# Optimization experiments

Hardware: AMD Instinct MI355X
Metric: run time of the kernel (lower is better)

The kernel has to match this reference:

```python
import jax, jax.numpy as jnp
import numpy as np

N = 100000          # num nodes
E = 1600000         # num edges (before self loops)
IN_C = 128
OUT_C = 64
RATIO = 0.5
NEG_SLOPE = 0.2


def setup_inputs() -> dict:
    key = jax.random.key(0)
    k1, k2, k3, k4, k5 = jax.random.split(key, 5)
    x = jax.random.normal(k1, (N, IN_C), jnp.float32)
    # edges with no self loops (module removes then re-adds self loops)
    src = jax.random.randint(k2, (E,), 0, N, dtype=jnp.int32)
    off = jax.random.randint(k3, (E,), 1, N, dtype=jnp.int32)
    tgt = (src + off) % N
    edge_index = jnp.stack([src, tgt])  # [2, E], row0=source(j), row1=target(i)
    # glorot init
    s_w = float(np.sqrt(6.0 / (IN_C + OUT_C)))
    weight = jax.random.uniform(k4, (IN_C, OUT_C), jnp.float32, -s_w, s_w)
    s_a = float(np.sqrt(6.0 / (1 + 2 * OUT_C)))
    att = jax.random.uniform(k5, (1, 2 * OUT_C), jnp.float32, -s_a, s_a)
    batch = jnp.zeros((N,), jnp.int32)  # single graph
    return {"x": x, "weight": weight, "att": att,
            "edge_index": edge_index, "batch": batch, "bn": 0}


def reference(x, weight, att, edge_index, batch, bn):
    # add self loops (static shapes: E + N edges)
    loops = jnp.arange(N, dtype=edge_index.dtype)
    src = jnp.concatenate([edge_index[0], loops])  # edge_index_j (source)
    tgt = jnp.concatenate([edge_index[1], loops])  # edge_index_i (target)

    h = x @ weight                      # [N, OUT_C]
    x_j = h[src]                        # [E+N, OUT_C] gathered source feats
    x_i = h[tgt]

    # alpha = (cat([x_i, x_j]) * att).sum(-1)
    alpha = x_i @ att[0, :OUT_C] + x_j @ att[0, OUT_C:]   # [E+N]
    alpha = jnp.where(alpha > 0, alpha, NEG_SLOPE * alpha)  # leaky_relu

    # edge-softmax grouped by target node (every node has a self loop -> no empty segment)
    m = jax.ops.segment_max(alpha, tgt, num_segments=N)
    a = jnp.exp(alpha - m[tgt])
    denom = jax.ops.segment_sum(a, tgt, num_segments=N)
    alpha = a / (denom[tgt] + 1e-16)

    # node importance = sum of attention over outgoing edges (grouped by source)
    alpha_sum = jax.ops.segment_sum(alpha, src, num_segments=N)

    # topk node selection (ratio of all nodes; single graph)
    k = int(np.ceil(RATIO * N))
    _, topk_idx = jax.lax.top_k(alpha_sum, k)
    node_mask = jnp.zeros((N,), bool).at[topk_idx].set(True)

    # filter_dn: keep edges whose both endpoints survive; mask instead of compacting
    edge_mask = node_mask[src] & node_mask[tgt]
    alpha_m = jnp.where(edge_mask, alpha, 0.0)

    # weighted scatter-add aggregation to target nodes (aggr='add')
    out = jax.ops.segment_sum(alpha_m[:, None] * x_j, tgt, num_segments=N)  # [N, OUT_C]
    # bn flag is 0 -> BatchNorm skipped
    return out, edge_mask, node_mask
```

## Files before the change

kernel.cpp:

```cpp
#include <hip/hip_runtime.h>
#include <stdint.h>

#define IN_C 128
#define OUT_C 64
#define NEG_SLOPE 0.2f
#define RB 256
#define RBINS 512
#define STAGE 8192
#define NGH (RBINS * RB)
#define NGHS (RBINS * RBINS)
#define KC 8
#define SXW 192

typedef unsigned int u32;
typedef unsigned long long u64;

__device__ __forceinline__ u32 fenc(float f) {
  u32 u = __float_as_uint(f);
  return (u & 0x80000000u) ? ~u : (u | 0x80000000u);
}
__device__ __forceinline__ u64 key64(float v, int i) {
  return (((u64)fenc(v)) << 32) | (u64)(0xffffffffu - (u32)i);
}

__global__ __launch_bounds__(128) void k_gemm(const float* __restrict__ x,
                                              const float* __restrict__ w,
                                              const float* __restrict__ att,
                                              float* __restrict__ h,
                                              float* __restrict__ ai, float* __restrict__ aj,
                                              int N) {
  __shared__ float sw[IN_C * OUT_C];
  __shared__ float sx[KC * SXW];
  int tid = threadIdx.x;
  int rbase = blockIdx.x * 128;

  for (int i = tid; i < (IN_C * OUT_C) / 4; i += 128)
    ((float4*)sw)[i] = ((const float4*)w)[i];

  int c0 = (tid & 7) * 8;
  int rg = tid >> 3;
  int sxbase = rg * 12;
  float acc[8][8];
#pragma unroll
  for (int i = 0; i < 8; i++)
#pragma unroll
    for (int j = 0; j < 8; j++) acc[i][j] = 0.f;

  int grow = rbase + tid;
  int base = (tid >> 3) * 12 + (tid & 7);
  const float* xp = &x[(size_t)grow * IN_C];

  float4 pv0 = make_float4(0.f, 0.f, 0.f, 0.f);
  float4 pv1 = make_float4(0.f, 0.f, 0.f, 0.f);
  if (grow < N) {
    pv0 = *(const float4*)&xp[0];
    pv1 = *(const float4*)&xp[4];
  }

  for (int kb = 0; kb < IN_C; kb += KC) {
    __syncthreads();
    sx[0 * SXW + base] = pv0.x;
    sx[1 * SXW + base] = pv0.y;
    sx[2 * SXW + base] = pv0.z;
    sx[3 * SXW + base] = pv0.w;
    sx[4 * SXW + base] = pv1.x;
    sx[5 * SXW + base] = pv1.y;
    sx[6 * SXW + base] = pv1.z;
    sx[7 * SXW + base] = pv1.w;
    if (kb + KC < IN_C && grow < N) {
      pv0 = *(const float4*)&xp[kb + KC];
      pv1 = *(const float4*)&xp[kb + KC + 4];
    }
    __syncthreads();
#pragma unroll
    for (int kl = 0; kl < KC; ++kl) {
      int kg = kb + kl;
      float xr[8], wv[8];
      *(float4*)&xr[0] = *(const float4*)&sx[kl * SXW + sxbase];
      *(float4*)&xr[4] = *(const float4*)&sx[kl * SXW + sxbase + 4];
      *(float4*)&wv[0] = *(const float4*)&sw[kg * OUT_C + c0];
      *(float4*)&wv[4] = *(const float4*)&sw[kg * OUT_C + c0 + 4];
#pragma unroll
      for (int i = 0; i < 8; ++i)
#pragma unroll
        for (int j = 0; j < 8; ++j)
          acc[i][j] += xr[i] * wv[j];
    }
  }

  float pi[8], pj[8];
#pragma unroll
  for (int i = 0; i < 8; ++i) { pi[i] = 0.f; pj[i] = 0.f; }
#pragma unroll
  for (int j = 0; j < 8; ++j) {
    float a0 = att[c0 + j], a1 = att[OUT_C + c0 + j];
#pragma unroll
    for (int i = 0; i < 8; ++i) {
      pi[i] += acc[i][j] * a0;
      pj[i] += acc[i][j] * a1;
    }
  }
#pragma unroll
  for (int o = 1; o < 8; o <<= 1) {
#pragma unroll
    for (int i = 0; i < 8; ++i) {
      pi[i] += __shfl_xor(pi[i], o);
      pj[i] += __shfl_xor(pj[i], o);
    }
  }
#pragma unroll
  for (int i = 0; i < 8; ++i) {
    int row = rbase + rg * 8 + i;
    if (row < N) {
      *(float4*)&h[(size_t)row * OUT_C + c0]     = make_float4(acc[i][0], acc[i][1], acc[i][2], acc[i][3]);
      *(float4*)&h[(size_t)row * OUT_C + c0 + 4] = make_float4(acc[i][4], acc[i][5], acc[i][6], acc[i][7]);
      if ((tid & 7) == 0) { ai[row] = pi[i]; aj[row] = pj[i]; }
    }
  }
}

__global__ __launch_bounds__(256) void k_rhist_t(const int* __restrict__ tgt,
                                                 int E, int EN, int chunk, u32* __restrict__ gh,
                                                 u32* __restrict__ hist8, u32* __restrict__ done,
                                                 u32* __restrict__ sel, u32* __restrict__ cnt, u32 k) {
  __shared__ u32 lh[RBINS];
  int tid = threadIdx.x, b = blockIdx.x;
  if (b == 0) {
    for (int i = tid; i < 2048; i += 256) hist8[i] = 0u;
    if (tid < 8) { done[tid] = 0u; cnt[tid] = 0u; }
    if (tid == 0) { sel[0] = 0u; sel[1] = 0u; sel[2] = k; sel[3] = 0u; }
  }
  for (int d = tid; d < RBINS; d += 256) lh[d] = 0u;
  __syncthreads();
  int lo = b * chunk, hi = min(lo + chunk, EN);
  for (int e = lo + tid; e < hi; e += 256) {
    int t = (e < E) ? tgt[e] : e - E;
    atomicAdd(&lh[((u32)t) >> 8], 1u);
  }
  __syncthreads();
  for (int d = tid; d < RBINS; d += 256) gh[d * RB + b] = lh[d];
}

__global__ __launch_bounds__(256) void k_scanA(const u32* __restrict__ in, u32* __restrict__ out,
                                               u32* __restrict__ bsum, int n) {
  __shared__ u32 s[256];
  int i = blockIdx.x * 256 + threadIdx.x;
  u32 v = (i < n) ? in[i] : 0u;
  s[threadIdx.x] = v;
  __syncthreads();
  for (int o = 1; o < 256; o <<= 1) {
    u32 t = (threadIdx.x >= (unsigned)o) ? s[threadIdx.x - o] : 0u;
    __syncthreads();
    s[threadIdx.x] += t;
    __syncthreads();
  }
  if (i < n) out[i] = s[threadIdx.x] - v;
  if (threadIdx.x == 255) bsum[blockIdx.x] = s[255];
}

__global__ __launch_bounds__(1024) void k_scanB(u32* __restrict__ bsum, int nb) {
  __shared__ u32 s[1024];
  int tid = threadIdx.x;
  u32 v = (tid < nb) ? bsum[tid] : 0u;
  s[tid] = v;
  __syncthreads();
  for (int o = 1; o < 1024; o <<= 1) {
    u32 t = (tid >= o) ? s[tid - o] : 0u;
    __syncthreads();
    s[tid] += t;
    __syncthreads();
  }
  if (tid < nb) bsum[tid] = s[tid] - v;
}

__global__ __launch_bounds__(256) void k_scanC(u32* __restrict__ out, const u32* __restrict__ bsum, int n) {
  int i = blockIdx.x * 256 + threadIdx.x;
  if (i < n) out[i] += bsum[blockIdx.x];
}

__global__ __launch_bounds__(256) void k_rscatter_t(const int* __restrict__ src, const int* __restrict__ tgt,
                                                    int E, int EN, int chunk,
                                                    const u32* __restrict__ gh, u32* __restrict__ bufB) {
  __shared__ u32 cnt[RBINS];
  int tid = threadIdx.x, b = blockIdx.x;
  for (int d = tid; d < RBINS; d += 256) cnt[d] = gh[d * RB + b];
  __syncthreads();
  int lo = b * chunk, hi = min(lo + chunk, EN);
  for (int e = lo + tid; e < hi; e += 256) {
    int s, t;
    if (e < E) { s = src[e]; t = tgt[e]; } else { s = t = e - E; }
    u32 p = atomicAdd(&cnt[((u32)t) >> 8], 1u);
    bufB[p] = (((u32)t & 255u) << 24) | (u32)s;
  }
}

__global__ __launch_bounds__(256) void k_rpass2(const u32* __restrict__ in, u32* __restrict__ out,
                                                const u32* __restrict__ gh, u32* __restrict__ ghs,
                                                u32* __restrict__ offT,
                                                const float* __restrict__ ai, const float* __restrict__ aj,
                                                float* __restrict__ alpha,
                                                int N, int EN) {
  __shared__ u32 hist[256];
  __shared__ u32 sc[256];
  __shared__ u32 lhs[RBINS];
  __shared__ u32 stage[STAGE];
  int tid = threadIdx.x, d = blockIdx.x;
  u32 start = gh[d * RB];
  u32 end = (d < RBINS - 1) ? gh[(d + 1) * RB] : (u32)EN;
  int sz = (int)(end - start);
  hist[tid] = 0u;
  for (int dd = tid; dd < RBINS; dd += 256) lhs[dd] = 0u;
  __syncthreads();
  for (u32 p = start + tid; p < end; p += 256) {
    u32 it = in[p];
    atomicAdd(&hist[it >> 24], 1u);
    atomicAdd(&lhs[(it & 0xffffffu) >> 8], 1u);
  }
  __syncthreads();
  for (int dd = tid; dd < RBINS; dd += 256) ghs[dd * RBINS + d] = lhs[dd];
  u32 hv = hist[tid];
  sc[tid] = hv;
  __syncthreads();
  for (int o = 1; o < 256; o <<= 1) {
    u32 t = (tid >= o) ? sc[tid - o] : 0u;
    __syncthreads();
    sc[tid] += t;
    __syncthreads();
  }
  u32 excl = sc[tid] - hv;
  int node = (d << 8) + tid;
  if (node < N) offT[node] = start + excl;
  if (node == 0) offT[N] = (u32)EN;
  hist[tid] = excl;
  __syncthreads();
  bool staged = (sz <= STAGE);
  for (u32 p = start + tid; p < end; p += 256) {
    u32 it = in[p];
    u32 lp = atomicAdd(&hist[it >> 24], 1u);
    if (staged) stage[lp] = it;
    else out[start + lp] = it;
  }
  __syncthreads();
  if (staged)
    for (int i = tid; i < sz; i += 256) out[start + i] = stage[i];
  __syncthreads();
  if (node < N) {
    int lb = (tid > 0) ? (int)sc[tid - 1] : 0;
    int le = (int)sc[tid];
    float an = ai[node];
    float mx = -1e30f;
    for (int i = lb; i < le; ++i) {
      u32 it = staged ? stage[i] : out[start + i];
      float a = an + aj[it & 0xffffffu];
      a = a > 0.f ? a : NEG_SLOPE * a;
      mx = fmaxf(mx, a);
      if (staged) stage[i] = __float_as_uint(a);
    }
    float sm = 0.f;
    for (int i = lb; i < le; ++i) {
      float a;
      if (staged) a = __uint_as_float(stage[i]);
      else {
        u32 it = out[start + i];
        a = an + aj[it & 0xffffffu];
        a = a > 0.f ? a : NEG_SLOPE * a;
      }
      float v = expf(a - mx);
      sm += v;
      if (staged) stage[i] = __float_as_uint(v);
      else alpha[start + i] = v;
    }
    float inv = 1.f / (sm + 1e-16f);
    for (int i = lb; i < le; ++i) {
      float v = staged ? __uint_as_float(stage[i]) : alpha[start + i];
      alpha[start + i] = v * inv;
    }
  }
}

__global__ __launch_bounds__(256) void k_rscatter_s(const u32* __restrict__ csr,
                                                    const float* __restrict__ alpha,
                                                    const u32* __restrict__ gh, const u32* __restrict__ ghs,
                                                    u64* __restrict__ bufB, int EN) {
  __shared__ u32 cnt[RBINS];
  int tid = threadIdx.x, d = blockIdx.x;
  for (int dd = tid; dd < RBINS; dd += 256) cnt[dd] = ghs[dd * RBINS + d];
  __syncthreads();
  u32 start = gh[d * RB];
  u32 end = (d < RBINS - 1) ? gh[(d + 1) * RB] : (u32)EN;
  for (u32 e = start + tid; e < end; e += 256) {
    u32 s = csr[e] & 0xffffffu;
    u32 p = atomicAdd(&cnt[s >> 8], 1u);
    bufB[p] = (((u64)(s & 255u)) << 32) | __float_as_uint(alpha[e]);
  }
}

__global__ __launch_bounds__(256) void k_asum_acc(const u64* __restrict__ bufB,
                                                  const u32* __restrict__ ghs,
                                                  float* __restrict__ asum, int N, int EN) {
  __shared__ float sums[256];
  int tid = threadIdx.x, d = blockIdx.x;
  u32 start = ghs[d * RBINS];
  u32 end = (d < RBINS - 1) ? ghs[(d + 1) * RBINS] : (u32)EN;
  sums[tid] = 0.f;
  __syncthreads();
  for (u32 p = start + tid; p < end; p += 256) {
    u64 it = bufB[p];
    atomicAdd(&sums[(u32)(it >> 32)], __uint_as_float((u32)it));
  }
  __syncthreads();
  int node = d * 256 + tid;
  if (node < N) asum[node] = sums[tid];
}

__global__ __launch_bounds__(256) void k_histpick(const float* __restrict__ asum,
                                                  const u32* __restrict__ list_in, const u32* __restrict__ cnt_in,
                                                  u32* __restrict__ list_out, u32* __restrict__ cnt_out,
                                                  u32* __restrict__ hist8, u32* __restrict__ done,
                                                  u32* __restrict__ sel, int N, int pass, int nblk) {
  __shared__ u32 lh[256];
  __shared__ u32 sres;
  __shared__ u32 s[256];
  int tid = threadIdx.x;
  lh[tid] = 0u;
  __syncthreads();
  u64 prefix = ((const u64*)sel)[0];
  int shift = 56 - 8 * pass;
  int n = list_in ? (int)*cnt_in : N;
  int i = blockIdx.x * 256 + tid;
  if (i < n) {
    int idx = list_in ? (int)list_in[i] : i;
    u64 k = key64(asum[idx], idx);
    bool ok = (pass == 0) || ((k >> (shift + 8)) == prefix);
    if (ok) {
      atomicAdd(&lh[(u32)(k >> shift) & 255u], 1u);
      if (list_out) {
        u32 p = atomicAdd(cnt_out, 1u);
        list_out[p] = (u32)idx;
      }
    }
  }
  __syncthreads();
  if (lh[tid]) atomicAdd(&hist8[pass * 256 + tid], lh[tid]);
  __syncthreads();
  if (tid == 0)
    sres = __hip_atomic_fetch_add(&done[pass], 1u, __ATOMIC_ACQ_REL, __HIP_MEMORY_SCOPE_AGENT);
  __syncthreads();
  if (sres == (u32)(nblk - 1)) {
    u32 krem = sel[2];
    u32 hv = __hip_atomic_load(&hist8[pass * 256 + (255 - tid)], __ATOMIC_RELAXED,
                               __HIP_MEMORY_SCOPE_AGENT);
    s[tid] = hv;
    __syncthreads();
    for (int o = 1; o < 256; o <<= 1) {
      u32 t = (tid >= o) ? s[tid - o] : 0u;
      __syncthreads();
      s[tid] += t;
      __syncthreads();
    }
    u32 cum = s[tid], prev = (tid > 0) ? s[tid - 1] : 0u;
    if (cum >= krem && prev < krem) {
      int dsel = 255 - tid;
      ((u64*)sel)[0] = (prefix << 8) | (u64)(u32)dsel;
      sel[2] = krem - prev;
    }
  }
}

__global__ __launch_bounds__(256) void k_finish(const float* __restrict__ asum,
                                                const u32* __restrict__ list, const u32* __restrict__ cntp,
                                                u32* __restrict__ sel) {
  __shared__ u64 keys[2048];
  __shared__ u32 cc;
  int tid = threadIdx.x;
  if (tid == 0) cc = 0u;
  __syncthreads();
  int n = (int)*cntp;
  u32 fsel = (u32)((const u64*)sel)[0];
  u32 krem = sel[2];
  for (int i = tid; i < n; i += 256) {
    int idx = (int)list[i];
    u64 k = key64(asum[idx], idx);
    if ((u32)(k >> 32) == fsel) {
      u32 p = atomicAdd(&cc, 1u);
      if (p < 2048) keys[p] = k;
    }
  }
  __syncthreads();
  int C = (int)min(cc, 2048u);
  for (int i = tid; i < C; i += 256) {
    u64 k = keys[i];
    u32 rank = 0;
    for (int j = 0; j < C; ++j)
      if (keys[j] > k) rank++;
    if (rank == krem - 1) ((u64*)sel)[0] = k;
  }
}

__global__ __launch_bounds__(256) void k_node_mask(const float* __restrict__ asum,
                                                   const u32* __restrict__ sel,
                                                   u32* __restrict__ nm,
                                                   float* __restrict__ out_node, int N) {
  int i = blockIdx.x * 256 + threadIdx.x;
  if (i >= N) return;
  u64 T = ((const u64*)sel)[0];
  bool m = key64(asum[i], i) >= T;
  nm[i] = m ? 1u : 0u;
  out_node[i] = m ? 1.f : 0.f;
}

__global__ __launch_bounds__(256) void k_mask(const int* __restrict__ src, const int* __restrict__ tgt,
                                              const u32* __restrict__ nm,
                                              const u32* __restrict__ csr, const float* __restrict__ alpha,
                                              float* __restrict__ out_edge, u64* __restrict__ pair,
                                              int E, int EN) {
  int e = blockIdx.x * 256 + threadIdx.x;
  if (e >= EN) return;
  int s, t;
  if (e < E) { s = src[e]; t = tgt[e]; } else { s = t = e - E; }
  out_edge[e] = (nm[s] && nm[t]) ? 1.f : 0.f;
  u32 sp = csr[e] & 0xffffffu;
  u32 ab = nm[sp] ? __float_as_uint(alpha[e]) : 0u;
  pair[e] = (((u64)sp) << 32) | ab;
}

__global__ __launch_bounds__(256) void k_aggregate(const u32* __restrict__ off,
                                                   const u64* __restrict__ pair,
                                                   const float* __restrict__ h,
                                                   const u32* __restrict__ nm,
                                                   float* __restrict__ out, int N) {
  int node = blockIdx.x * 4 + (threadIdx.x >> 6);
  int lane = threadIdx.x & 63;
  int g = lane >> 4;
  int c = lane & 15;
  if (node >= N) return;
  float4 acc = make_float4(0.f, 0.f, 0.f, 0.f);
  if (nm[node]) {
    u32 b = off[node], e2 = off[node + 1];
    for (u32 p0 = b; p0 < e2; p0 += 16) {
      u64 pr[4];
      float av[4];
      u32 sv[4];
#pragma unroll
      for (int q = 0; q < 4; ++q) {
        u32 p = p0 + q * 4 + (u32)g;
        bool ok = p < e2;
        pr[q] = pair[ok ? p : b];
        av[q] = ok ? __uint_as_float((u32)pr[q]) : 0.f;
        sv[q] = (u32)(pr[q] >> 32);
      }
      float4 hv[4];
#pragma unroll
      for (int q = 0; q < 4; ++q)
        hv[q] = *(const float4*)&h[(size_t)sv[q] * OUT_C + c * 4];
#pragma unroll
      for (int q = 0; q < 4; ++q) {
        acc.x += av[q] * hv[q].x;
        acc.y += av[q] * hv[q].y;
        acc.z += av[q] * hv[q].z;
        acc.w += av[q] * hv[q].w;
      }
    }
#pragma unroll
    for (int o = 16; o < 64; o <<= 1) {
      acc.x += __shfl_xor(acc.x, o);
      acc.y += __shfl_xor(acc.y, o);
      acc.z += __shfl_xor(acc.z, o);
      acc.w += __shfl_xor(acc.w, o);
    }
  }
  if (g == 0)
    *(float4*)&out[(size_t)node * OUT_C + c * 4] = acc;
}

extern "C" void kernel_launch(void* const* d_in, const int* in_sizes, int n_in,
                              void* d_out, int out_size, void* d_ws, size_t ws_size,
                              hipStream_t stream) {
  const float* x   = (const float*)d_in[0];
  const float* w   = (const float*)d_in[1];
  const float* att = (const float*)d_in[2];
  const int*   ei  = (const int*)d_in[3];

  int N = in_sizes[0] / IN_C;
  int E = in_sizes[3] / 2;
  int EN = E + N;
  const int* src = ei;
  const int* tgt = ei + E;

  float* out      = (float*)d_out;
  float* out_edge = out + (size_t)N * OUT_C;
  float* out_node = out_edge + (size_t)EN;

  char* p = (char*)d_ws;
  auto alloc = [&](size_t bytes) -> char* {
    char* r = p;
    p += (bytes + 255) & ~(size_t)255;
    return r;
  };
  float* h     = (float*)alloc((size_t)N * OUT_C * 4);
  float* ai    = (float*)alloc((size_t)N * 4);
  float* aj    = (float*)alloc((size_t)N * 4);
  u32*   bufA  = (u32*)alloc((size_t)EN * 4);
  u64*   bufB  = (u64*)alloc((size_t)EN * 8);
  float* alpha = (float*)alloc((size_t)EN * 4);
  u32*   offT  = (u32*)alloc((size_t)(N + 1) * 4);
  u32*   gh    = (u32*)alloc((size_t)NGH * 4);
  u32*   ghs   = (u32*)alloc((size_t)NGHS * 4);
  u32*   bsum  = (u32*)alloc(2048 * 4);
  float* asum  = (float*)alloc((size_t)N * 4);
  u32*   nm    = (u32*)alloc((size_t)N * 4);
  u32*   hist8 = (u32*)alloc(2048 * 4);
  u32*   done  = (u32*)alloc(8 * 4);
  u32*   cnt   = (u32*)alloc(8 * 4);
  u32*   sel   = (u32*)alloc(256);
  u32*   listA = (u32*)alloc((size_t)N * 4);
  u32*   listB = (u32*)alloc((size_t)N * 4);

  u32 kSel = (u32)((N + 1) / 2);
  int chunk = (EN + RB - 1) / RB;
  int nScanT = (NGH + 255) / 256;
  int nScanS = (NGHS + 255) / 256;
  int gGemm = (N + 127) / 128;
  int gN = (N + 255) / 256;
  int gE = (EN + 255) / 256;
  int gNode4 = (N + 3) / 4;

  k_gemm<<<gGemm, 128, 0, stream>>>(x, w, att, h, ai, aj, N);

  k_rhist_t<<<RB, 256, 0, stream>>>(tgt, E, EN, chunk, gh, hist8, done, sel, cnt, kSel);
  k_scanA<<<nScanT, 256, 0, stream>>>(gh, gh, bsum, NGH);
  k_scanB<<<1, 1024, 0, stream>>>(bsum, nScanT);
  k_scanC<<<nScanT, 256, 0, stream>>>(gh, bsum, NGH);
  k_rscatter_t<<<RB, 256, 0, stream>>>(src, tgt, E, EN, chunk, gh, (u32*)bufB);
  k_rpass2<<<RBINS, 256, 0, stream>>>((u32*)bufB, bufA, gh, ghs, offT, ai, aj, alpha, N, EN);

  k_scanA<<<nScanS, 256, 0, stream>>>(ghs, ghs, bsum, NGHS);
  k_scanB<<<1, 1024, 0, stream>>>(bsum, nScanS);
  k_scanC<<<nScanS, 256, 0, stream>>>(ghs, bsum, NGHS);
  k_rscatter_s<<<RBINS, 256, 0, stream>>>(bufA, alpha, gh, ghs, bufB, EN);
  k_asum_acc<<<RBINS, 256, 0, stream>>>(bufB, ghs, asum, N, EN);

  k_histpick<<<gN, 256, 0, stream>>>(asum, nullptr, nullptr, nullptr, nullptr,
                                     hist8, done, sel, N, 0, gN);
  k_histpick<<<gN, 256, 0, stream>>>(asum, nullptr, nullptr, listA, &cnt[1],
                                     hist8, done, sel, N, 1, gN);
  k_histpick<<<gN, 256, 0, stream>>>(asum, listA, &cnt[1], listB, &cnt[2],
                                     hist8, done, sel, N, 2, gN);
  k_histpick<<<gN, 256, 0, stream>>>(asum, listB, &cnt[2], listA, &cnt[3],
                                     hist8, done, sel, N, 3, gN);
  k_finish<<<1, 256, 0, stream>>>(asum, listA, &cnt[3], sel);

  k_node_mask<<<gN, 256, 0, stream>>>(asum, sel, nm, out_node, N);
  k_mask<<<gE, 256, 0, stream>>>(src, tgt, nm, bufA, alpha, out_edge, bufB, E, EN);
  k_aggregate<<<gNode4, 256, 0, stream>>>(offT, bufB, h, nm, out, N);
}
```

Before: 365.6 us.

## Replace source-side radix sort with global atomic accumulation of attention sums

```diff
diff --git a/kernel.cpp b/kernel.cpp
--- a/kernel.cpp
+++ b/kernel.cpp
@@ -8,7 +8,6 @@
 #define RBINS 512
 #define STAGE 8192
 #define NGH (RBINS * RB)
-#define NGHS (RBINS * RBINS)
 #define KC 8
 #define SXW 192
 
@@ -122,7 +121,8 @@
 __global__ __launch_bounds__(256) void k_rhist_t(const int* __restrict__ tgt,
                                                  int E, int EN, int chunk, u32* __restrict__ gh,
                                                  u32* __restrict__ hist8, u32* __restrict__ done,
-                                                 u32* __restrict__ sel, u32* __restrict__ cnt, u32 k) {
+                                                 u32* __restrict__ sel, u32* __restrict__ cnt, u32 k,
+                                                 float* __restrict__ asum, int N) {
   __shared__ u32 lh[RBINS];
   int tid = threadIdx.x, b = blockIdx.x;
   if (b == 0) {
@@ -130,6 +130,11 @@
     if (tid < 8) { done[tid] = 0u; cnt[tid] = 0u; }
     if (tid == 0) { sel[0] = 0u; sel[1] = 0u; sel[2] = k; sel[3] = 0u; }
   }
+  {
+    int per = (N + RB - 1) / RB;
+    int z0 = b * per, z1 = min(z0 + per, N);
+    for (int i = z0 + tid; i < z1; i += 256) asum[i] = 0.f;
+  }
   for (int d = tid; d < RBINS; d += 256) lh[d] = 0u;
   __syncthreads();
   int lo = b * chunk, hi = min(lo + chunk, EN);
@@ -195,29 +200,25 @@
 }
 
 __global__ __launch_bounds__(256) void k_rpass2(const u32* __restrict__ in, u32* __restrict__ out,
-                                                const u32* __restrict__ gh, u32* __restrict__ ghs,
+                                                const u32* __restrict__ gh,
                                                 u32* __restrict__ offT,
                                                 const float* __restrict__ ai, const float* __restrict__ aj,
-                                                float* __restrict__ alpha,
+                                                float* __restrict__ alpha, float* __restrict__ asum,
                                                 int N, int EN) {
   __shared__ u32 hist[256];
   __shared__ u32 sc[256];
-  __shared__ u32 lhs[RBINS];
   __shared__ u32 stage[STAGE];
   int tid = threadIdx.x, d = blockIdx.x;
   u32 start = gh[d * RB];
   u32 end = (d < RBINS - 1) ? gh[(d + 1) * RB] : (u32)EN;
   int sz = (int)(end - start);
   hist[tid] = 0u;
-  for (int dd = tid; dd < RBINS; dd += 256) lhs[dd] = 0u;
   __syncthreads();
   for (u32 p = start + tid; p < end; p += 256) {
     u32 it = in[p];
     atomicAdd(&hist[it >> 24], 1u);
-    atomicAdd(&lhs[(it & 0xffffffu) >> 8], 1u);
-  }
-  __syncthreads();
-  for (int dd = tid; dd < RBINS; dd += 256) ghs[dd * RBINS + d] = lhs[dd];
+  }
+  __syncthreads();
   u32 hv = hist[tid];
   sc[tid] = hv;
   __syncthreads();
@@ -272,45 +273,12 @@
     }
     float inv = 1.f / (sm + 1e-16f);
     for (int i = lb; i < le; ++i) {
-      float v = staged ? __uint_as_float(stage[i]) : alpha[start + i];
-      alpha[start + i] = v * inv;
-    }
-  }
-}
-
-__global__ __launch_bounds__(256) void k_rscatter_s(const u32* __restrict__ csr,
-                                                    const float* __restrict__ alpha,
-                                                    const u32* __restrict__ gh, const u32* __restrict__ ghs,
-                                                    u64* __restrict__ bufB, int EN) {
-  __shared__ u32 cnt[RBINS];
-  int tid = threadIdx.x, d = blockIdx.x;
-  for (int dd = tid; dd < RBINS; dd += 256) cnt[dd] = ghs[dd * RBINS + d];
-  __syncthreads();
-  u32 start = gh[d * RB];
-  u32 end = (d < RBINS - 1) ? gh[(d + 1) * RB] : (u32)EN;
-  for (u32 e = start + tid; e < end; e += 256) {
-    u32 s = csr[e] & 0xffffffu;
-    u32 p = atomicAdd(&cnt[s >> 8], 1u);
-    bufB[p] = (((u64)(s & 255u)) << 32) | __float_as_uint(alpha[e]);
-  }
-}
-
-__global__ __launch_bounds__(256) void k_asum_acc(const u64* __restrict__ bufB,
-                                                  const u32* __restrict__ ghs,
-                                                  float* __restrict__ asum, int N, int EN) {
-  __shared__ float sums[256];
-  int tid = threadIdx.x, d = blockIdx.x;
-  u32 start = ghs[d * RBINS];
-  u32 end = (d < RBINS - 1) ? ghs[(d + 1) * RBINS] : (u32)EN;
-  sums[tid] = 0.f;
-  __syncthreads();
-  for (u32 p = start + tid; p < end; p += 256) {
-    u64 it = bufB[p];
-    atomicAdd(&sums[(u32)(it >> 32)], __uint_as_float((u32)it));
-  }
-  __syncthreads();
-  int node = d * 256 + tid;
-  if (node < N) asum[node] = sums[tid];
+      float v = (staged ? __uint_as_float(stage[i]) : alpha[start + i]) * inv;
+      alpha[start + i] = v;
+      u32 sp = out[start + i] & 0xffffffu;
+      atomicAdd(&asum[sp], v);
+    }
+  }
 }
 
 __global__ __launch_bounds__(256) void k_histpick(const float* __restrict__ asum,
@@ -451,8 +419,11 @@
       }
       float4 hv[4];
 #pragma unroll
-      for (int q = 0; q < 4; ++q)
-        hv[q] = *(const float4*)&h[(size_t)sv[q] * OUT_C + c * 4];
+      for (int q = 0; q < 4; ++q) {
+        hv[q] = make_float4(0.f, 0.f, 0.f, 0.f);
+        if (av[q] != 0.f)
+          hv[q] = *(const float4*)&h[(size_t)sv[q] * OUT_C + c * 4];
+      }
 #pragma unroll
       for (int q = 0; q < 4; ++q) {
         acc.x += av[q] * hv[q].x;
@@ -505,7 +476,6 @@
   float* alpha = (float*)alloc((size_t)EN * 4);
   u32*   offT  = (u32*)alloc((size_t)(N + 1) * 4);
   u32*   gh    = (u32*)alloc((size_t)NGH * 4);
-  u32*   ghs   = (u32*)alloc((size_t)NGHS * 4);
   u32*   bsum  = (u32*)alloc(2048 * 4);
   float* asum  = (float*)alloc((size_t)N * 4);
   u32*   nm    = (u32*)alloc((size_t)N * 4);
@@ -519,7 +489,6 @@
   u32 kSel = (u32)((N + 1) / 2);
   int chunk = (EN + RB - 1) / RB;
   int nScanT = (NGH + 255) / 256;
-  int nScanS = (NGHS + 255) / 256;
   int gGemm = (N + 127) / 128;
   int gN = (N + 255) / 256;
   int gE = (EN + 255) / 256;
@@ -527,18 +496,12 @@
 
   k_gemm<<<gGemm, 128, 0, stream>>>(x, w, att, h, ai, aj, N);
 
-  k_rhist_t<<<RB, 256, 0, stream>>>(tgt, E, EN, chunk, gh, hist8, done, sel, cnt, kSel);
+  k_rhist_t<<<RB, 256, 0, stream>>>(tgt, E, EN, chunk, gh, hist8, done, sel, cnt, kSel, asum, N);
   k_scanA<<<nScanT, 256, 0, stream>>>(gh, gh, bsum, NGH);
   k_scanB<<<1, 1024, 0, stream>>>(bsum, nScanT);
   k_scanC<<<nScanT, 256, 0, stream>>>(gh, bsum, NGH);
   k_rscatter_t<<<RB, 256, 0, stream>>>(src, tgt, E, EN, chunk, gh, (u32*)bufB);
-  k_rpass2<<<RBINS, 256, 0, stream>>>((u32*)bufB, bufA, gh, ghs, offT, ai, aj, alpha, N, EN);
-
-  k_scanA<<<nScanS, 256, 0, stream>>>(ghs, ghs, bsum, NGHS);
-  k_scanB<<<1, 1024, 0, stream>>>(bsum, nScanS);
-  k_scanC<<<nScanS, 256, 0, stream>>>(ghs, bsum, NGHS);
-  k_rscatter_s<<<RBINS, 256, 0, stream>>>(bufA, alpha, gh, ghs, bufB, EN);
-  k_asum_acc<<<RBINS, 256, 0, stream>>>(bufB, ghs, asum, N, EN);
+  k_rpass2<<<RBINS, 256, 0, stream>>>((u32*)bufB, bufA, gh, offT, ai, aj, alpha, asum, N, EN);
 
   k_histpick<<<gN, 256, 0, stream>>>(asum, nullptr, nullptr, nullptr, nullptr,
                                      hist8, done, sel, N, 0, gN);
```

Measured after the change: 408.8 us. +11.8%, slower.

## Fuse first top-k histogram pass into asum kernel and drop packed edge pairs

Applied to the files above, without the earlier changes.

```diff
diff --git a/kernel.cpp b/kernel.cpp
--- a/kernel.cpp
+++ b/kernel.cpp
@@ -297,8 +297,14 @@
 
 __global__ __launch_bounds__(256) void k_asum_acc(const u64* __restrict__ bufB,
                                                   const u32* __restrict__ ghs,
-                                                  float* __restrict__ asum, int N, int EN) {
+                                                  float* __restrict__ asum,
+                                                  u32* __restrict__ hist8, u32* __restrict__ done,
+                                                  u32* __restrict__ sel,
+                                                  int N, int EN, int nblk) {
   __shared__ float sums[256];
+  __shared__ u32 lh[256];
+  __shared__ u32 s[256];
+  __shared__ u32 sres;
   int tid = threadIdx.x, d = blockIdx.x;
   u32 start = ghs[d * RBINS];
   u32 end = (d < RBINS - 1) ? ghs[(d + 1) * RBINS] : (u32)EN;
@@ -310,7 +316,39 @@
   }
   __syncthreads();
   int node = d * 256 + tid;
-  if (node < N) asum[node] = sums[tid];
+  u32 bin = 256u;
+  if (node < N) {
+    float v = sums[tid];
+    asum[node] = v;
+    bin = (u32)(key64(v, node) >> 56) & 255u;
+  }
+  lh[tid] = 0u;
+  __syncthreads();
+  if (bin < 256u) atomicAdd(&lh[bin], 1u);
+  __syncthreads();
+  if (lh[tid]) atomicAdd(&hist8[tid], lh[tid]);
+  __syncthreads();
+  if (tid == 0)
+    sres = __hip_atomic_fetch_add(&done[0], 1u, __ATOMIC_ACQ_REL, __HIP_MEMORY_SCOPE_AGENT);
+  __syncthreads();
+  if (sres == (u32)(nblk - 1)) {
+    u32 krem = sel[2];
+    u32 hv = __hip_atomic_load(&hist8[255 - tid], __ATOMIC_RELAXED, __HIP_MEMORY_SCOPE_AGENT);
+    s[tid] = hv;
+    __syncthreads();
+    for (int o = 1; o < 256; o <<= 1) {
+      u32 t = (tid >= o) ? s[tid - o] : 0u;
+      __syncthreads();
+      s[tid] += t;
+      __syncthreads();
+    }
+    u32 cum = s[tid], prev = (tid > 0) ? s[tid - 1] : 0u;
+    if (cum >= krem && prev < krem) {
+      int dsel = 255 - tid;
+      ((u64*)sel)[0] = (u64)(u32)dsel;
+      sel[2] = krem - prev;
+    }
+  }
 }
 
 __global__ __launch_bounds__(256) void k_histpick(const float* __restrict__ asum,
@@ -411,21 +449,18 @@
 
 __global__ __launch_bounds__(256) void k_mask(const int* __restrict__ src, const int* __restrict__ tgt,
                                               const u32* __restrict__ nm,
-                                              const u32* __restrict__ csr, const float* __restrict__ alpha,
-                                              float* __restrict__ out_edge, u64* __restrict__ pair,
+                                              float* __restrict__ out_edge,
                                               int E, int EN) {
   int e = blockIdx.x * 256 + threadIdx.x;
   if (e >= EN) return;
   int s, t;
   if (e < E) { s = src[e]; t = tgt[e]; } else { s = t = e - E; }
   out_edge[e] = (nm[s] && nm[t]) ? 1.f : 0.f;
-  u32 sp = csr[e] & 0xffffffu;
-  u32 ab = nm[sp] ? __float_as_uint(alpha[e]) : 0u;
-  pair[e] = (((u64)sp) << 32) | ab;
 }
 
 __global__ __launch_bounds__(256) void k_aggregate(const u32* __restrict__ off,
-                                                   const u64* __restrict__ pair,
+                                                   const u32* __restrict__ csr,
+                                                   const float* __restrict__ alpha,
                                                    const float* __restrict__ h,
                                                    const u32* __restrict__ nm,
                                                    float* __restrict__ out, int N) {
@@ -438,21 +473,25 @@
   if (nm[node]) {
     u32 b = off[node], e2 = off[node + 1];
     for (u32 p0 = b; p0 < e2; p0 += 16) {
-      u64 pr[4];
       float av[4];
       u32 sv[4];
 #pragma unroll
       for (int q = 0; q < 4; ++q) {
         u32 p = p0 + q * 4 + (u32)g;
         bool ok = p < e2;
-        pr[q] = pair[ok ? p : b];
-        av[q] = ok ? __uint_as_float((u32)pr[q]) : 0.f;
-        sv[q] = (u32)(pr[q] >> 32);
+        u32 pp = ok ? p : b;
+        u32 sp = csr[pp] & 0xffffffu;
+        float a = alpha[pp];
+        sv[q] = sp;
+        av[q] = (ok && nm[sp]) ? a : 0.f;
       }
       float4 hv[4];
 #pragma unroll
-      for (int q = 0; q < 4; ++q)
-        hv[q] = *(const float4*)&h[(size_t)sv[q] * OUT_C + c * 4];
+      for (int q = 0; q < 4; ++q) {
+        hv[q] = make_float4(0.f, 0.f, 0.f, 0.f);
+        if (av[q] != 0.f)
+          hv[q] = *(const float4*)&h[(size_t)sv[q] * OUT_C + c * 4];
+      }
 #pragma unroll
       for (int q = 0; q < 4; ++q) {
         acc.x += av[q] * hv[q].x;
@@ -538,10 +577,8 @@
   k_scanB<<<1, 1024, 0, stream>>>(bsum, nScanS);
   k_scanC<<<nScanS, 256, 0, stream>>>(ghs, bsum, NGHS);
   k_rscatter_s<<<RBINS, 256, 0, stream>>>(bufA, alpha, gh, ghs, bufB, EN);
-  k_asum_acc<<<RBINS, 256, 0, stream>>>(bufB, ghs, asum, N, EN);
-
-  k_histpick<<<gN, 256, 0, stream>>>(asum, nullptr, nullptr, nullptr, nullptr,
-                                     hist8, done, sel, N, 0, gN);
+  k_asum_acc<<<RBINS, 256, 0, stream>>>(bufB, ghs, asum, hist8, done, sel, N, EN, RBINS);
+
   k_histpick<<<gN, 256, 0, stream>>>(asum, nullptr, nullptr, listA, &cnt[1],
                                      hist8, done, sel, N, 1, gN);
   k_histpick<<<gN, 256, 0, stream>>>(asum, listA, &cnt[1], listB, &cnt[2],
@@ -551,6 +588,6 @@
   k_finish<<<1, 256, 0, stream>>>(asum, listA, &cnt[3], sel);
 
   k_node_mask<<<gN, 256, 0, stream>>>(asum, sel, nm, out_node, N);
-  k_mask<<<gE, 256, 0, stream>>>(src, tgt, nm, bufA, alpha, out_edge, bufB, E, EN);
-  k_aggregate<<<gNode4, 256, 0, stream>>>(offT, bufB, h, nm, out, N);
-}
+  k_mask<<<gE, 256, 0, stream>>>(src, tgt, nm, out_edge, E, EN);
+  k_aggregate<<<gNode4, 256, 0, stream>>>(offT, bufA, alpha, h, nm, out, N);
+}
```

After: 362.4 us. About the same (-0.9%).
